# Kernel tuning notes

Hardware: AMD Instinct MI355X
Metric: run time of the kernel (lower is better)

Reference implementation:

```python
import jax, jax.numpy as jnp
import numpy as np

D_MODEL = 256
SEQ_L = 4096
BATCH = 8
H = 3 * D_MODEL   # inner width after 3-branch concat
N_STATE = 32      # complex conjugate pairs -> d_state=64 real
KSIZES = (3, 7, 15)
DILATIONS = (1, 2, 4)


def setup_inputs() -> dict:
    k = jax.random.split(jax.random.key(0), 16)
    d = D_MODEL
    def w(ki, shape, scale):
        return jax.random.normal(ki, shape, jnp.float32) * scale
    inp = {"x": jax.random.normal(k[0], (BATCH, SEQ_L, d), jnp.float32)}
    for i, ksz in enumerate(KSIZES):
        inp[f"conv_w{i}"] = w(k[1 + i], (d, d, ksz), (d * ksz) ** -0.5)
        inp[f"conv_b{i}"] = jnp.zeros((d,), jnp.float32)
    inp["gate_w"] = w(k[4], (H, d), d ** -0.5)
    inp["gate_b"] = jnp.zeros((H,), jnp.float32)
    inp["res_w"] = w(k[5], (H, d), d ** -0.5)
    inp["res_b"] = jnp.zeros((H,), jnp.float32)
    # S4D (diagonal SSM) parameters, d_state=64 -> 32 complex pairs
    inp["log_dt"] = jax.random.uniform(k[6], (H,), jnp.float32, np.log(0.001), np.log(0.1))
    inp["A_re"] = -0.5 * jnp.ones((H, N_STATE), jnp.float32)
    inp["A_im"] = jnp.broadcast_to(np.pi * jnp.arange(N_STATE, dtype=jnp.float32), (H, N_STATE)).copy()
    inp["C_re"] = w(k[7], (H, N_STATE), 0.2)
    inp["C_im"] = w(k[8], (H, N_STATE), 0.2)
    inp["Dskip"] = jax.random.normal(k[9], (H,), jnp.float32)
    inp["ln_gamma"] = jnp.ones((H,), jnp.float32)
    inp["ln_beta"] = jnp.zeros((H,), jnp.float32)
    return inp


def _dil_conv(u, w, b, dil):
    # u: [B, C, L], w: [O, I, K], torch 'same' padding (odd kernels)
    y = jax.lax.conv_general_dilated(
        u, w, window_strides=(1,), padding="SAME", rhs_dilation=(dil,),
        dimension_numbers=("NCH", "OIH", "NCH"))
    return y + b[None, :, None]


def _s4d_apply(u, log_dt, A_re, A_im, C_re, C_im, Dskip):
    # u: [B, H, L]; diagonal SSM long convolution via FFT (ZOH discretization)
    L = u.shape[-1]
    dt = jnp.exp(log_dt)                          # [H]
    A = A_re + 1j * A_im                          # [H, N]
    C = C_re + 1j * C_im                          # [H, N]
    dtA = dt[:, None] * A                         # [H, N]
    C_disc = C * (jnp.exp(dtA) - 1.0) / A         # ZOH input matrix folded into C
    t = jnp.arange(L, dtype=jnp.float32)
    vand = jnp.exp(dtA[:, :, None] * t)           # [H, N, L] Vandermonde
    kern = 2.0 * jnp.real(jnp.einsum("hn,hnl->hl", C_disc, vand))  # [H, L]
    n_fft = 2 * L
    kf = jnp.fft.rfft(kern, n_fft)                # [H, n_fft/2+1]
    uf = jnp.fft.rfft(u, n_fft)                   # [B, H, n_fft/2+1]
    y = jnp.fft.irfft(uf * kf[None], n_fft)[..., :L]
    return y + Dskip[None, :, None] * u


def reference(x, conv_w0, conv_b0, conv_w1, conv_b1, conv_w2, conv_b2,
              gate_w, gate_b, res_w, res_b,
              log_dt, A_re, A_im, C_re, C_im, Dskip, ln_gamma, ln_beta):
    u = jnp.transpose(x, (0, 2, 1))               # [B, d, L]
    convs = [
        _dil_conv(u, conv_w0, conv_b0, DILATIONS[0]),
        _dil_conv(u, conv_w1, conv_b1, DILATIONS[1]),
        _dil_conv(u, conv_w2, conv_b2, DILATIONS[2]),
    ]
    combined = jnp.concatenate(convs, axis=1)     # [B, 3d, L]
    gate = jax.nn.sigmoid(jnp.einsum("bdl,od->bol", u, gate_w) + gate_b[None, :, None])
    gated = combined * gate
    s4_out = _s4d_apply(gated, log_dt, A_re, A_im, C_re, C_im, Dskip)
    resid = jnp.einsum("bdl,od->bol", u, res_w) + res_b[None, :, None]
    out = jnp.transpose(s4_out + resid, (0, 2, 1))  # [B, L, 3d]
    mu = jnp.mean(out, axis=-1, keepdims=True)
    var = jnp.mean((out - mu) ** 2, axis=-1, keepdims=True)
    return (out - mu) * jax.lax.rsqrt(var + 1e-5) * ln_gamma + ln_beta
```

## Files before the change

kernel.cpp:

```cpp
#include <hip/hip_runtime.h>
#include <cstdint>
#include <cstddef>


#define B_ 8
#define L_ 4096
#define D_ 256
#define H_ 768
#define NST 32
#define LC 128
#define NC 32

typedef _Float16 f16;
typedef _Float16 f16x8 __attribute__((ext_vector_type(8)));
typedef _Float16 f16x4 __attribute__((ext_vector_type(4)));
typedef _Float16 f16x2 __attribute__((ext_vector_type(2)));
typedef float f32x4 __attribute__((ext_vector_type(4)));

__device__ __forceinline__ f32x4 mfma16(f16x8 a, f16x8 b, f32x4 c) {
  return __builtin_amdgcn_mfma_f32_16x16x32_f16(a, b, c, 0, 0, 0);
}

#define GLDS16(g, l)                                                              \
  __builtin_amdgcn_global_load_lds((const __attribute__((address_space(1))) void*)(g), \
                                   (__attribute__((address_space(3))) void*)(l), 16, 0, 0)

__global__ __launch_bounds__(256) void prep_all(
    const float* __restrict__ x, const float* __restrict__ gate_w,
    const float* __restrict__ res_w,
    const float* __restrict__ w0, const float* __restrict__ w1, const float* __restrict__ w2,
    f16* __restrict__ xh, f16* __restrict__ Ag, float* __restrict__ zbuf,
    f16* __restrict__ A) {
  __shared__ float ws_t[3840];
  int bid = blockIdx.x, tid = threadIdx.x;
  if (bid < 8192) {
    int i = (bid * 256 + tid) * 4;
    float4 v = *(const float4*)(x + i);
    f16x4 h; h[0]=(f16)v.x; h[1]=(f16)v.y; h[2]=(f16)v.z; h[3]=(f16)v.w;
    *(f16x4*)(xh + i) = h;
  } else if (bid < 8384) {
    int i = ((bid - 8192) * 256 + tid) * 4;
    float4 v = *(const float4*)(gate_w + i);
    f16x4 h; h[0]=(f16)v.x; h[1]=(f16)v.y; h[2]=(f16)v.z; h[3]=(f16)v.w;
    *(f16x4*)(Ag + i) = h;
  } else if (bid < 8576) {
    int i = ((bid - 8384) * 256 + tid) * 4;
    float4 v = *(const float4*)(res_w + i);
    f16* d = Ag + 768 * 256;
    f16x4 h; h[0]=(f16)v.x; h[1]=(f16)v.y; h[2]=(f16)v.z; h[3]=(f16)v.w;
    *(f16x4*)(d + i) = h;
  } else if (bid == 8576) {
    zbuf[tid] = 0.f;
  } else {
    int b2 = bid - 8577;
    int ci = b2 >> 8, o = b2 & 255;
    const float* w; int K, base;
    if (ci == 0)      { w = w0; K = 3;  base = 0; }
    else if (ci == 1) { w = w1; K = 7;  base = 256 * 768; }
    else              { w = w2; K = 15; base = 256 * 768 + 256 * 1792; }
    const float* wbase = w + (size_t)o * 256 * K;
    int n = 256 * K;
    for (int i = tid; i < n; i += 256) ws_t[i] = wbase[i];
    __syncthreads();
    f16* Ab = A + base + (size_t)o * 256 * K;
    for (int t = 0; t < K; ++t)
      Ab[t * 256 + tid] = (f16)ws_t[tid * K + t];
  }
}

__global__ __launch_bounds__(256) void s4_all(const float* __restrict__ log_dt,
                                              const float* __restrict__ A_re,
                                              const float* __restrict__ A_im,
                                              const float* __restrict__ C_re,
                                              const float* __restrict__ C_im,
                                              f16* __restrict__ A1, f16* __restrict__ A2,
                                              float* __restrict__ WLc,
                                              float* __restrict__ kT) {
  int bid = blockIdx.x, tid = threadIdx.x;
  if (bid < 96) {
    int idx = bid * 256 + tid;
    int h = idx >> 5, n = idx & 31;
    float dt = expf(log_dt[h]);
    float Ar = A_re[idx], Ai = A_im[idx];
    float ar = dt * Ar, ai = dt * Ai;
    float e = expf(ar), sn, cs; sincosf(ai, &sn, &cs);
    float wr = e * cs, wi = e * sn;
    float den = Ar * Ar + Ai * Ai;
    float Er = wr - 1.f, Ei = wi;
    float Cr = C_re[idx], Ci = C_im[idx];
    float nr = Cr * Er - Ci * Ei, ni = Cr * Ei + Ci * Er;
    float Cdr = (nr * Ar + ni * Ai) / den;
    float Cdi = (ni * Ar - nr * Ai) / den;
    f16* A1r = A1 + ((size_t)h * 64 + 2 * n) * LC;
    f16* A1i = A1 + ((size_t)h * 64 + 2 * n + 1) * LC;
    float pr = 1.f, pi = 0.f;
    for (int j = 0; j < LC; ++j) {
      A1r[LC - 1 - j] = (f16)pr; A1i[LC - 1 - j] = (f16)pi;
      float t0 = pr * wr - pi * wi; pi = pr * wi + pi * wr; pr = t0;
    }
    WLc[idx * 2] = pr; WLc[idx * 2 + 1] = pi;
    float qr = wr, qi = wi;
    for (int t = 0; t < LC; ++t) {
      A2[((size_t)h * LC + t) * 64 + 2 * n]     = (f16)(2.f * (Cdr * qr - Cdi * qi));
      A2[((size_t)h * LC + t) * 64 + 2 * n + 1] = (f16)(-2.f * (Cdr * qi + Cdi * qr));
      float t0 = qr * wr - qi * wi; qi = qr * wi + qi * wr; qr = t0;
    }
  } else {
    int idx = (bid - 96) * 256 + tid;
    int h = idx >> 7, j = idx & 127;
    float dt = expf(log_dt[h]);
    float acc = 0.f;
    for (int n = 0; n < NST; ++n) {
      float Ar = A_re[h * 32 + n], Ai = A_im[h * 32 + n];
      float ar = dt * Ar, ai = dt * Ai;
      float e1 = expf(ar), s1, c1; sincosf(ai, &s1, &c1);
      float wr = e1 * c1, wi = e1 * s1;
      float den = Ar * Ar + Ai * Ai;
      float Er = wr - 1.f, Ei = wi;
      float Cr = C_re[h * 32 + n], Ci = C_im[h * 32 + n];
      float nr = Cr * Er - Ci * Ei, ni = Cr * Ei + Ci * Er;
      float Cdr = (nr * Ar + ni * Ai) / den, Cdi = (ni * Ar - nr * Ai) / den;
      float ej = expf(ar * (float)j), sj, cj; sincosf(ai * (float)j, &sj, &cj);
      acc += 2.f * (Cdr * (ej * cj) - Cdi * (ej * sj));
    }
    kT[idx] = acc;
  }
}

__global__ __launch_bounds__(256) void gemm_gr(
    const f16* __restrict__ xh, const f16* __restrict__ Agr,
    const float* __restrict__ gate_b, const float* __restrict__ res_b,
    f16* __restrict__ gts, f16* __restrict__ res) {
  __shared__ f16 As[128 * 64];
  __shared__ f16 Bs[128 * 64];
  const int mt = blockIdx.y, nt = blockIdx.x;
  const int b = nt >> 5, l0 = (nt & 31) * 128;
  const bool isg = mt < 6;
  const int hbase = (isg ? mt : mt - 6) * 128;
  const f16* Abase = Agr + (size_t)((isg ? 0 : 768) + hbase) * 256;
  const int tid = threadIdx.x;
  const int wid = tid >> 6, lane = tid & 63, l15 = lane & 15, quad = lane >> 4;
  const int wm = (wid & 1) * 64, wn = (wid >> 1) * 64;
  const int srow = (wid << 5) + (lane >> 3);
  const int sperm = ((lane & 7) ^ (lane >> 3)) << 3;
  char* AsL = (char*)As + (wid << 12);
  char* BsL = (char*)Bs + (wid << 12);
  const f16* xrow = xh + (((size_t)b * L_) << 8);

  f32x4 acc[4][4];
#pragma unroll
  for (int i = 0; i < 4; ++i)
#pragma unroll
    for (int j = 0; j < 4; ++j) acc[i][j] = (f32x4){0.f, 0.f, 0.f, 0.f};

  for (int kc = 0; kc < 4; ++kc) {
#pragma unroll
    for (int j = 0; j < 4; ++j) {
      int row = srow + j * 8;
      GLDS16(Abase + (size_t)row * 256 + kc * 64 + sperm, AsL + (j << 10));
      GLDS16(xrow + ((size_t)(l0 + row) << 8) + kc * 64 + sperm, BsL + (j << 10));
    }
    __syncthreads();
#pragma unroll
    for (int k2 = 0; k2 < 2; ++k2) {
      f16x8 af[4], bf[4];
#pragma unroll
      for (int mi = 0; mi < 4; ++mi) {
        int r = wm + mi * 16 + l15;
        af[mi] = *(const f16x8*)(&As[r * 64 + (((k2 * 4 + quad) ^ (r & 7)) << 3)]);
      }
#pragma unroll
      for (int ni = 0; ni < 4; ++ni) {
        int r = wn + ni * 16 + l15;
        bf[ni] = *(const f16x8*)(&Bs[r * 64 + (((k2 * 4 + quad) ^ (r & 7)) << 3)]);
      }
#pragma unroll
      for (int mi = 0; mi < 4; ++mi)
#pragma unroll
        for (int ni = 0; ni < 4; ++ni) acc[mi][ni] = mfma16(af[mi], bf[ni], acc[mi][ni]);
    }
    __syncthreads();
  }

  if (isg) {
#pragma unroll
    for (int mi = 0; mi < 4; ++mi)
#pragma unroll
      for (int ni = 0; ni < 4; ++ni) {
        int hg = hbase + wm + mi * 16 + quad * 4;
        int lg = l0 + wn + ni * 16 + l15;
#pragma unroll
        for (int r = 0; r < 4; ++r) {
          float val = acc[mi][ni][r] + gate_b[hg + r];
          gts[((size_t)(b * H_ + hg + r)) * L_ + lg] = (f16)(1.f / (1.f + expf(-val)));
        }
      }
  } else {
#pragma unroll
    for (int mi = 0; mi < 4; ++mi)
#pragma unroll
      for (int ni = 0; ni < 4; ++ni) {
        int hg = hbase + wm + mi * 16 + quad * 4;
        int lg = l0 + wn + ni * 16 + l15;
#pragma unroll
        for (int r = 0; r < 4; ++r)
          res[((size_t)(b * H_ + hg + r)) * L_ + lg] = (f16)(acc[mi][ni][r] + res_b[hg + r]);
      }
  }
}

__global__ __launch_bounds__(512, 2) void gemm_conv8(
    const f16* __restrict__ xh, const f16* __restrict__ Aconv,
    const float* __restrict__ cb0, const float* __restrict__ cb1, const float* __restrict__ cb2,
    const f16* __restrict__ gts, const f16* __restrict__ zbuf,
    f16* __restrict__ v) {
  __shared__ f16 lds[69632];
  f16* Bs = lds + 49152;

  const int nt = blockIdx.x;
  const int b = nt >> 4, l0 = (nt & 15) * 256;
  const int ci = 2 - blockIdx.y;
  const int tid = threadIdx.x;
  const int wid = tid >> 6, lane = tid & 63, l15 = lane & 15, quad = lane >> 4;
  const int wr = wid >> 1, wc = wid & 1;
  const int rq = tid >> 3;
  const int cswz = ((tid & 7) ^ ((tid >> 3) & 7)) << 3;
  const f16* xrow = xh + (((size_t)b * L_) << 8);

  const f16* Acb; int Krow, taps, dil;
  if (ci == 0)      { Acb = Aconv;                          Krow = 768;  taps = 3;  dil = 1; }
  else if (ci == 1) { Acb = Aconv + 256 * 768;              Krow = 1792; taps = 7;  dil = 2; }
  else              { Acb = Aconv + 256 * 768 + 256 * 1792; Krow = 3840; taps = 15; dil = 4; }
  const int half = (taps - 1) / 2;
  const int shift0 = 32 - half * dil;

  f32x4 acc[4][8];
#pragma unroll
  for (int i = 0; i < 4; ++i)
#pragma unroll
    for (int j = 0; j < 8; ++j) acc[i][j] = (f32x4){0.f, 0.f, 0.f, 0.f};
  f16x8 af[4][2], bfA[2][2], bfB[2][2];

  auto stageB = [&](int jc) {
#pragma unroll
    for (int q = 0; q < 5; ++q) {
      int r = q * 64 + rq;
      int gl = l0 - 32 + r;
      const f16* src = (gl < 0 || gl >= L_) ? (zbuf + cswz)
                       : xrow + ((size_t)gl << 8) + jc * 64 + cswz;
      GLDS16(src, Bs + q * 4096 + wid * 512);
    }
  };
  auto stageA4 = [&](int t2, int jc2, f16* buf) {
#pragma unroll
    for (int q = 0; q < 4; ++q) {
      const f16* src = Acb + (size_t)(q * 64 + rq) * Krow + t2 * 256 + jc2 * 64 + cswz;
      GLDS16(src, buf + q * 4096 + wid * 512);
    }
  };
  auto readAF = [&](const f16* Ab) {
#pragma unroll
    for (int mi = 0; mi < 4; ++mi) {
      int r = wr * 64 + mi * 16 + l15;
#pragma unroll
      for (int k2 = 0; k2 < 2; ++k2)
        af[mi][k2] = *(const f16x8*)(Ab + r * 64 + (((k2 * 4 + quad) ^ (r & 7)) << 3));
    }
  };
  auto readBF = [&](int q, int shift, f16x8 (&bf)[2][2]) {
#pragma unroll
    for (int ni = 0; ni < 2; ++ni) {
      int r = shift + wc * 128 + q * 32 + ni * 16 + l15;
#pragma unroll
      for (int k2 = 0; k2 < 2; ++k2)
        bf[ni][k2] = *(const f16x8*)(Bs + r * 64 + (((k2 * 4 + quad) ^ (r & 7)) << 3));
    }
  };
  auto qMM = [&](int q, f16x8 (&bf)[2][2]) {
#pragma unroll
    for (int k2 = 0; k2 < 2; ++k2)
#pragma unroll
      for (int mi = 0; mi < 4; ++mi)
#pragma unroll
        for (int ni = 0; ni < 2; ++ni)
          acc[mi][q * 2 + ni] = mfma16(af[mi][k2], bf[ni][k2], acc[mi][q * 2 + ni]);
  };

  stageB(0);
  stageA4(0, 0, lds);
  stageA4(1, 0, lds + 16384);
  asm volatile("s_waitcnt vmcnt(0)" ::: "memory");
  __builtin_amdgcn_s_barrier();
  readBF(0, shift0, bfA);

  int ca = 0;
#pragma unroll 1
  for (int jc = 0; jc < 4; ++jc) {
#pragma unroll 1
    for (int t = 0; t < taps; ++t) {
      const int shift = shift0 + t * dil;
      f16* Acur = lds + ca * 16384;
      int pa = ca + 2; if (pa >= 3) pa -= 3;
      f16* Apre = lds + pa * 16384;
      int t2 = t + 2, jc2 = jc;
      if (t2 >= taps) { t2 -= taps; ++jc2; }
      const bool pf = (jc2 < 4);

      if (pf) stageA4(t2, jc2, Apre);
      readAF(Acur);
      readBF(1, shift, bfB);
      qMM(0, bfA);
      readBF(2, shift, bfA);
      qMM(1, bfB);
      readBF(3, shift, bfB);
      qMM(2, bfA);
      qMM(3, bfB);

      if (t < taps - 1) {
        readBF(0, shift + dil, bfA);
        if (pf) asm volatile("s_waitcnt vmcnt(4)" ::: "memory");
        else    asm volatile("s_waitcnt vmcnt(0)" ::: "memory");
        __builtin_amdgcn_s_barrier();
      } else if (jc < 3) {
        __builtin_amdgcn_s_barrier();
        stageB(jc + 1);
        asm volatile("s_waitcnt vmcnt(0)" ::: "memory");
        __builtin_amdgcn_s_barrier();
        readBF(0, shift0, bfA);
      }
      ca = (ca == 2) ? 0 : ca + 1;
    }
  }

  const float* cbias = (ci == 0) ? cb0 : (ci == 1 ? cb1 : cb2);
#pragma unroll
  for (int mi = 0; mi < 4; ++mi)
#pragma unroll
    for (int q = 0; q < 4; ++q)
#pragma unroll
      for (int ni = 0; ni < 2; ++ni) {
        int mg = wr * 64 + mi * 16 + quad * 4;
        int lg = l0 + wc * 128 + q * 32 + ni * 16 + l15;
        f32x4 a4 = acc[mi][q * 2 + ni];
#pragma unroll
        for (int r = 0; r < 4; ++r) {
          size_t a = ((size_t)(b * H_ + ci * 256 + mg + r)) * L_ + lg;
          float val = (a4[r] + cbias[mg + r]) * (float)gts[a];
          v[a] = (f16)val;
        }
      }
}

__global__ __launch_bounds__(256) void s1_states(const f16* __restrict__ v,
                                                 const f16* __restrict__ A1,
                                                 const float* __restrict__ WLc,
                                                 f16* __restrict__ Xin) {
  __shared__ f16 A1s[64 * 136];
  __shared__ f16 Vs[128 * 136];
  const int h = blockIdx.y, cb = blockIdx.x;
  const int tid = threadIdx.x;
  {
    int row = tid >> 2, q = tid & 3;
    const f16x8* src = (const f16x8*)(A1 + ((size_t)h * 64 + row) * 128 + q * 32);
    f16x8* dst = (f16x8*)(&A1s[row * 136 + q * 32]);
    dst[0] = src[0]; dst[1] = src[1]; dst[2] = src[2]; dst[3] = src[3];
  }
  {
    int col = tid >> 1, half = tid & 1;
    int cg = cb * 128 + col, b = cg >> 5, c = cg & 31;
    const f16x8* src = (const f16x8*)(v + ((size_t)(b * H_ + h)) * L_ + c * 128 + half * 64);
    f16x8* dst = (f16x8*)(&Vs[col * 136 + half * 64]);
    dst[0] = src[0]; dst[1] = src[1]; dst[2] = src[2]; dst[3] = src[3];
    dst[4] = src[4]; dst[5] = src[5]; dst[6] = src[6]; dst[7] = src[7];
  }
  __syncthreads();
  const int wid = tid >> 6, lane = tid & 63, l15 = lane & 15, quad = lane >> 4;
  const int n0 = wid * 32;
  f32x4 acc[4][2];
#pragma unroll
  for (int i = 0; i < 4; ++i) { acc[i][0] = (f32x4){0,0,0,0}; acc[i][1] = (f32x4){0,0,0,0}; }
#pragma unroll
  for (int bk = 0; bk < 4; ++bk) {
    f16x8 af[4], bf[2];
#pragma unroll
    for (int mi = 0; mi < 4; ++mi)
      af[mi] = *(const f16x8*)(&A1s[(mi * 16 + l15) * 136 + bk * 32 + quad * 8]);
#pragma unroll
    for (int ni = 0; ni < 2; ++ni)
      bf[ni] = *(const f16x8*)(&Vs[(n0 + ni * 16 + l15) * 136 + bk * 32 + quad * 8]);
#pragma unroll
    for (int mi = 0; mi < 4; ++mi)
#pragma unroll
      for (int ni = 0; ni < 2; ++ni) acc[mi][ni] = mfma16(af[mi], bf[ni], acc[mi][ni]);
  }
  __syncthreads();
  float* Xls = (float*)Vs;
#pragma unroll
  for (int mi = 0; mi < 4; ++mi)
#pragma unroll
    for (int ni = 0; ni < 2; ++ni) {
      int col = n0 + ni * 16 + l15;
      *(f32x4*)(&Xls[col * 68 + mi * 16 + quad * 4]) = acc[mi][ni];
    }
  __syncthreads();
  if (tid < 128) {
    int b4 = tid >> 5, n = tid & 31;
    int b = cb * 4 + b4;
    float Wr = WLc[(h * NST + n) * 2], Wi = WLc[(h * NST + n) * 2 + 1];
    float xr = 0.f, xi = 0.f;
    f16* xout = Xin + (((size_t)(b * H_ + h)) * NC) * 64 + 2 * n;
    for (int c = 0; c < NC; ++c) {
      float er = Xls[(b4 * 32 + c) * 68 + 2 * n];
      float ei = Xls[(b4 * 32 + c) * 68 + 2 * n + 1];
      f16x2 o; o[0] = (f16)xr; o[1] = (f16)xi;
      *(f16x2*)(xout + (size_t)c * 64) = o;
      float t = Wr * xr - Wi * xi + er;
      xi = Wr * xi + Wi * xr + ei; xr = t;
    }
  }
}

__global__ __launch_bounds__(256) void s3_output(const f16* __restrict__ v,
                                                 const f16* __restrict__ A2g,
                                                 const f16* __restrict__ res,
                                                 const float* __restrict__ kT,
                                                 const f16* __restrict__ Xin,
                                                 const float* __restrict__ Dskip,
                                                 f16* __restrict__ y4) {
  __shared__ f16 Ts[128 * 136];
  __shared__ f16 Vs[64 * 136];
  __shared__ float kTs[128];
  f16* A2s = Ts;
  f16* Xs = Ts + 128 * 72;
  const int h = blockIdx.y, cb = blockIdx.x;
  const int tid = threadIdx.x;
  if (tid < 128) kTs[tid] = kT[h * 128 + tid];
  {
    int col = tid >> 2, q = tid & 3;
    int cg = cb * 64 + col, b = cg >> 5, c = cg & 31;
    const f16x8* src = (const f16x8*)(v + ((size_t)(b * H_ + h)) * L_ + c * 128 + q * 32);
    f16x8* dst = (f16x8*)(&Vs[col * 136 + q * 32]);
    dst[0] = src[0]; dst[1] = src[1]; dst[2] = src[2]; dst[3] = src[3];
  }
  __syncthreads();
  {
    int tau = tid >> 1, h64 = (tid & 1) * 64;
#pragma unroll
    for (int jv = 0; jv < 8; ++jv) {
      int s0 = h64 + jv * 8;
      f16x8 w;
#pragma unroll
      for (int e = 0; e < 8; ++e) {
        int s = s0 + e;
        w[e] = (f16)((s <= tau) ? kTs[tau - s] : 0.f);
      }
      *(f16x8*)(&Ts[tau * 136 + s0]) = w;
    }
  }
  __syncthreads();
  const int wid = tid >> 6, lane = tid & 63, l15 = lane & 15, quad = lane >> 4;
  const int wm = (wid & 1) * 64, wn = (wid >> 1) * 32;
  f32x4 acc[4][2];
#pragma unroll
  for (int i = 0; i < 4; ++i) { acc[i][0] = (f32x4){0,0,0,0}; acc[i][1] = (f32x4){0,0,0,0}; }
#pragma unroll
  for (int bk = 0; bk < 4; ++bk) {
    f16x8 af[4], bf[2];
#pragma unroll
    for (int mi = 0; mi < 4; ++mi)
      af[mi] = *(const f16x8*)(&Ts[(wm + mi * 16 + l15) * 136 + bk * 32 + quad * 8]);
#pragma unroll
    for (int ni = 0; ni < 2; ++ni)
      bf[ni] = *(const f16x8*)(&Vs[(wn + ni * 16 + l15) * 136 + bk * 32 + quad * 8]);
#pragma unroll
    for (int mi = 0; mi < 4; ++mi)
#pragma unroll
      for (int ni = 0; ni < 2; ++ni) acc[mi][ni] = mfma16(af[mi], bf[ni], acc[mi][ni]);
  }
  __syncthreads();
  {
    int row = tid >> 1, half = tid & 1;
    const f16x8* src = (const f16x8*)(A2g + ((size_t)h * 128 + row) * 64 + half * 32);
    f16x8* dst = (f16x8*)(&A2s[row * 72 + half * 32]);
    dst[0] = src[0]; dst[1] = src[1]; dst[2] = src[2]; dst[3] = src[3];
  }
  {
    int col = tid >> 2, part = tid & 3;
    int cg = cb * 64 + col, b = cg >> 5, c = cg & 31;
    const f16x8* src = (const f16x8*)(Xin + (((size_t)(b * H_ + h)) * NC + c) * 64 + part * 16);
    f16x8* dst = (f16x8*)(&Xs[col * 72 + part * 16]);
    dst[0] = src[0]; dst[1] = src[1];
  }
  __syncthreads();
#pragma unroll
  for (int bk = 0; bk < 2; ++bk) {
    f16x8 af[4], bf[2];
#pragma unroll
    for (int mi = 0; mi < 4; ++mi)
      af[mi] = *(const f16x8*)(&A2s[(wm + mi * 16 + l15) * 72 + bk * 32 + quad * 8]);
#pragma unroll
    for (int ni = 0; ni < 2; ++ni)
      bf[ni] = *(const f16x8*)(&Xs[(wn + ni * 16 + l15) * 72 + bk * 32 + quad * 8]);
#pragma unroll
    for (int mi = 0; mi < 4; ++mi)
#pragma unroll
      for (int ni = 0; ni < 2; ++ni) acc[mi][ni] = mfma16(af[mi], bf[ni], acc[mi][ni]);
  }
  float Dh = Dskip[h];
#pragma unroll
  for (int mi = 0; mi < 4; ++mi)
#pragma unroll
    for (int ni = 0; ni < 2; ++ni) {
      int col = wn + ni * 16 + l15;
      int cg = cb * 64 + col, b = cg >> 5, c = cg & 31;
      int tau0 = wm + mi * 16 + quad * 4;
      size_t lbase = ((size_t)(b * H_ + h)) * L_ + c * 128 + tau0;
      const f16* rp = res + lbase;
      f16x4 o;
#pragma unroll
      for (int r = 0; r < 4; ++r)
        o[r] = (f16)(acc[mi][ni][r] + Dh * (float)Vs[col * 136 + tau0 + r] + (float)rp[r]);
      *(f16x4*)(y4 + lbase) = o;
    }
}

__global__ __launch_bounds__(256) void layernorm_t(const f16* __restrict__ y4,
                                                   const float* __restrict__ gamma,
                                                   const float* __restrict__ beta,
                                                   float* __restrict__ out) {
  __shared__ f16 Ys[768 * 66];
  __shared__ float psum[256], psq[256], mu[64], rs[64];
  const int b = blockIdx.y, l0 = blockIdx.x * 64;
  const int tid = threadIdx.x;
  {
    int r8 = tid >> 3, c = tid & 7;
    for (int it = 0; it < 24; ++it) {
      int hh = it * 32 + r8;
      f16x8 x = *(const f16x8*)(y4 + ((size_t)(b * H_ + hh)) * L_ + l0 + c * 8);
      *(f16x8*)(&Ys[hh * 66 + c * 8]) = x;
    }
  }
  __syncthreads();
  {
    int l = tid & 63, hg = tid >> 6;
    float s = 0.f, s2 = 0.f;
    for (int k = 0; k < 192; ++k) {
      float val = (float)Ys[(hg * 192 + k) * 66 + l];
      s += val; s2 += val * val;
    }
    psum[hg * 64 + l] = s; psq[hg * 64 + l] = s2;
  }
  __syncthreads();
  if (tid < 64) {
    float S = 0.f, S2 = 0.f;
    for (int g = 0; g < 4; ++g) { S += psum[g * 64 + tid]; S2 += psq[g * 64 + tid]; }
    float m = S / 768.f;
    float var = S2 / 768.f - m * m;
    mu[tid] = m; rs[tid] = rsqrtf(var + 1e-5f);
  }
  __syncthreads();
  float g0 = gamma[tid], g1 = gamma[256 + tid], g2 = gamma[512 + tid];
  float be0 = beta[tid], be1 = beta[256 + tid], be2 = beta[512 + tid];
  for (int lv = 0; lv < 8; ++lv) {
    f16x8 y0 = *(const f16x8*)(&Ys[(size_t)tid * 66 + lv * 8]);
    f16x8 y1 = *(const f16x8*)(&Ys[(size_t)(256 + tid) * 66 + lv * 8]);
    f16x8 y2 = *(const f16x8*)(&Ys[(size_t)(512 + tid) * 66 + lv * 8]);
#pragma unroll
    for (int e = 0; e < 8; ++e) {
      int ll = lv * 8 + e;
      float m = mu[ll], r = rs[ll];
      size_t ob = ((size_t)b * L_ + l0 + ll) * H_;
      out[ob + tid]       = ((float)y0[e] - m) * r * g0 + be0;
      out[ob + 256 + tid] = ((float)y1[e] - m) * r * g1 + be1;
      out[ob + 512 + tid] = ((float)y2[e] - m) * r * g2 + be2;
    }
  }
}

extern "C" void kernel_launch(void* const* d_in, const int* in_sizes, int n_in,
                              void* d_out, int out_size, void* d_ws, size_t ws_size,
                              hipStream_t stream) {
  const float* x      = (const float*)d_in[0];
  const float* cw0    = (const float*)d_in[1];
  const float* cb0    = (const float*)d_in[2];
  const float* cw1    = (const float*)d_in[3];
  const float* cb1    = (const float*)d_in[4];
  const float* cw2    = (const float*)d_in[5];
  const float* cb2    = (const float*)d_in[6];
  const float* gate_w = (const float*)d_in[7];
  const float* gate_b = (const float*)d_in[8];
  const float* res_w  = (const float*)d_in[9];
  const float* res_b  = (const float*)d_in[10];
  const float* log_dt = (const float*)d_in[11];
  const float* A_re   = (const float*)d_in[12];
  const float* A_im   = (const float*)d_in[13];
  const float* C_re   = (const float*)d_in[14];
  const float* C_im   = (const float*)d_in[15];
  const float* Dskip  = (const float*)d_in[16];
  const float* ln_g   = (const float*)d_in[17];
  const float* ln_b   = (const float*)d_in[18];
  float* out = (float*)d_out;

  char* ws = (char*)d_ws;
  f16*   xh   = (f16*)(ws + 0);
  f16*   Ac   = (f16*)(ws + 16777216);
  f16*   Ag   = (f16*)(ws + 20054016);
  f16*   zbuf = (f16*)(ws + 20840448);
  f16*   vb   = (f16*)(ws + 20841472);
  f16*   resb = (f16*)(ws + 71173120);
  f16*   gts  = (f16*)(ws + 121504768);
  f16*   A1   = (f16*)(ws + 171836416);
  f16*   A2   = (f16*)(ws + 184419328);
  float* kT   = (float*)(ws + 197002240);
  float* WLc  = (float*)(ws + 197395456);
  f16*   Xin  = (f16*)(ws + 197592064);
  f16*   y4   = (f16*)(ws + 222757888);

  prep_all<<<9345, 256, 0, stream>>>(x, gate_w, res_w, cw0, cw1, cw2,
                                     xh, Ag, (float*)zbuf, Ac);
  s4_all<<<480, 256, 0, stream>>>(log_dt, A_re, A_im, C_re, C_im, A1, A2, WLc, kT);

  gemm_gr<<<dim3(256, 12), 256, 0, stream>>>(xh, Ag, gate_b, res_b, gts, resb);
  gemm_conv8<<<dim3(128, 3), 512, 0, stream>>>(xh, Ac, cb0, cb1, cb2, gts, zbuf, vb);

  s1_states<<<dim3(2, 768), 256, 0, stream>>>(vb, A1, WLc, Xin);
  s3_output<<<dim3(4, 768), 256, 0, stream>>>(vb, A2, resb, kT, Xin, Dskip, y4);

  layernorm_t<<<dim3(64, 8), 256, 0, stream>>>(y4, ln_g, ln_b, out);
}
```

Before: 445.5 us.

## Fuse gate GEMM and sigmoid into conv GEMM kernel, drop gate buffer

Moves the gate projection GEMM out of gemm_gr and into the conv kernel. Each conv block first computes the gate tile for its own channels and positions, applies the sigmoid and keeps the result in registers as f16, then runs the conv taps and multiplies by the gate in its epilogue. This removes a write and a read of the B*H*L f16 gate tensor in global memory and halves the gemm_gr grid. The cost is extra registers per thread for the held gate values and a gate pre-pass with full barriers before the conv pipeline starts, which could hurt occupancy under launch_bounds(512,2).

```diff
diff --git a/kernel.cpp b/kernel.cpp
--- a/kernel.cpp
+++ b/kernel.cpp
@@ -129,15 +129,13 @@
 
 __global__ __launch_bounds__(256) void gemm_gr(
     const f16* __restrict__ xh, const f16* __restrict__ Agr,
-    const float* __restrict__ gate_b, const float* __restrict__ res_b,
-    f16* __restrict__ gts, f16* __restrict__ res) {
+    const float* __restrict__ res_b, f16* __restrict__ res) {
   __shared__ f16 As[128 * 64];
   __shared__ f16 Bs[128 * 64];
   const int mt = blockIdx.y, nt = blockIdx.x;
   const int b = nt >> 5, l0 = (nt & 31) * 128;
-  const bool isg = mt < 6;
-  const int hbase = (isg ? mt : mt - 6) * 128;
-  const f16* Abase = Agr + (size_t)((isg ? 0 : 768) + hbase) * 256;
+  const int hbase = mt * 128;
+  const f16* Abase = Agr + (size_t)(768 + hbase) * 256;
   const int tid = threadIdx.x;
   const int wid = tid >> 6, lane = tid & 63, l15 = lane & 15, quad = lane >> 4;
   const int wm = (wid & 1) * 64, wn = (wid >> 1) * 64;
@@ -182,37 +180,23 @@
     __syncthreads();
   }
 
-  if (isg) {
-#pragma unroll
-    for (int mi = 0; mi < 4; ++mi)
-#pragma unroll
-      for (int ni = 0; ni < 4; ++ni) {
-        int hg = hbase + wm + mi * 16 + quad * 4;
-        int lg = l0 + wn + ni * 16 + l15;
-#pragma unroll
-        for (int r = 0; r < 4; ++r) {
-          float val = acc[mi][ni][r] + gate_b[hg + r];
-          gts[((size_t)(b * H_ + hg + r)) * L_ + lg] = (f16)(1.f / (1.f + expf(-val)));
-        }
-      }
-  } else {
-#pragma unroll
-    for (int mi = 0; mi < 4; ++mi)
-#pragma unroll
-      for (int ni = 0; ni < 4; ++ni) {
-        int hg = hbase + wm + mi * 16 + quad * 4;
-        int lg = l0 + wn + ni * 16 + l15;
-#pragma unroll
-        for (int r = 0; r < 4; ++r)
-          res[((size_t)(b * H_ + hg + r)) * L_ + lg] = (f16)(acc[mi][ni][r] + res_b[hg + r]);
-      }
-  }
-}
-
-__global__ __launch_bounds__(512, 2) void gemm_conv8(
+#pragma unroll
+  for (int mi = 0; mi < 4; ++mi)
+#pragma unroll
+    for (int ni = 0; ni < 4; ++ni) {
+      int hg = hbase + wm + mi * 16 + quad * 4;
+      int lg = l0 + wn + ni * 16 + l15;
+#pragma unroll
+      for (int r = 0; r < 4; ++r)
+        res[((size_t)(b * H_ + hg + r)) * L_ + lg] = (f16)(acc[mi][ni][r] + res_b[hg + r]);
+    }
+}
+
+__global__ __launch_bounds__(512, 2) void gemm_convg(
     const f16* __restrict__ xh, const f16* __restrict__ Aconv,
+    const f16* __restrict__ Agate,
     const float* __restrict__ cb0, const float* __restrict__ cb1, const float* __restrict__ cb2,
-    const f16* __restrict__ gts, const f16* __restrict__ zbuf,
+    const float* __restrict__ gate_b, const f16* __restrict__ zbuf,
     f16* __restrict__ v) {
   __shared__ f16 lds[69632];
   f16* Bs = lds + 49152;
@@ -258,6 +242,13 @@
       GLDS16(src, buf + q * 4096 + wid * 512);
     }
   };
+  auto stageAg = [&](int jc2, f16* buf) {
+#pragma unroll
+    for (int q = 0; q < 4; ++q) {
+      const f16* src = Agate + (size_t)(ci * 256 + q * 64 + rq) * 256 + jc2 * 64 + cswz;
+      GLDS16(src, buf + q * 4096 + wid * 512);
+    }
+  };
   auto readAF = [&](const f16* Ab) {
 #pragma unroll
     for (int mi = 0; mi < 4; ++mi) {
@@ -286,7 +277,35 @@
           acc[mi][q * 2 + ni] = mfma16(af[mi][k2], bf[ni][k2], acc[mi][q * 2 + ni]);
   };
 
-  stageB(0);
+#pragma unroll 1
+  for (int u = 0; u < 4; ++u) {
+    int jcs = (u + 1) & 3;
+    stageB(jcs);
+    stageAg(jcs, lds);
+    asm volatile("s_waitcnt vmcnt(0)" ::: "memory");
+    __builtin_amdgcn_s_barrier();
+    readAF(lds);
+    readBF(0, 32, bfA); qMM(0, bfA);
+    readBF(1, 32, bfB); qMM(1, bfB);
+    readBF(2, 32, bfA); qMM(2, bfA);
+    readBF(3, 32, bfB); qMM(3, bfB);
+    __builtin_amdgcn_s_barrier();
+  }
+  f16x4 g4[4][8];
+#pragma unroll
+  for (int mi = 0; mi < 4; ++mi)
+#pragma unroll
+    for (int j = 0; j < 8; ++j) {
+      int mg = wr * 64 + mi * 16 + quad * 4;
+      f32x4 a4 = acc[mi][j];
+#pragma unroll
+      for (int r = 0; r < 4; ++r) {
+        float gv = a4[r] + gate_b[ci * 256 + mg + r];
+        g4[mi][j][r] = (f16)(1.f / (1.f + expf(-gv)));
+      }
+      acc[mi][j] = (f32x4){0.f, 0.f, 0.f, 0.f};
+    }
+
   stageA4(0, 0, lds);
   stageA4(1, 0, lds + 16384);
   asm volatile("s_waitcnt vmcnt(0)" ::: "memory");
@@ -345,7 +364,7 @@
 #pragma unroll
         for (int r = 0; r < 4; ++r) {
           size_t a = ((size_t)(b * H_ + ci * 256 + mg + r)) * L_ + lg;
-          float val = (a4[r] + cbias[mg + r]) * (float)gts[a];
+          float val = (a4[r] + cbias[mg + r]) * (float)g4[mi][q * 2 + ni][r];
           v[a] = (f16)val;
         }
       }
@@ -608,7 +627,6 @@
   f16*   zbuf = (f16*)(ws + 20840448);
   f16*   vb   = (f16*)(ws + 20841472);
   f16*   resb = (f16*)(ws + 71173120);
-  f16*   gts  = (f16*)(ws + 121504768);
   f16*   A1   = (f16*)(ws + 171836416);
   f16*   A2   = (f16*)(ws + 184419328);
   float* kT   = (float*)(ws + 197002240);
@@ -620,8 +638,9 @@
                                      xh, Ag, (float*)zbuf, Ac);
   s4_all<<<480, 256, 0, stream>>>(log_dt, A_re, A_im, C_re, C_im, A1, A2, WLc, kT);
 
-  gemm_gr<<<dim3(256, 12), 256, 0, stream>>>(xh, Ag, gate_b, res_b, gts, resb);
-  gemm_conv8<<<dim3(128, 3), 512, 0, stream>>>(xh, Ac, cb0, cb1, cb2, gts, zbuf, vb);
+  gemm_gr<<<dim3(256, 6), 256, 0, stream>>>(xh, Ag, res_b, resb);
+  gemm_convg<<<dim3(128, 3), 512, 0, stream>>>(xh, Ac, Ag, cb0, cb1, cb2,
+                                               gate_b, zbuf, vb);
 
   s1_states<<<dim3(2, 768), 256, 0, stream>>>(vb, A1, WLc, Xin);
   s3_output<<<dim3(4, 768), 256, 0, stream>>>(vb, A2, resb, kT, Xin, Dskip, y4);
```

Measured after the change: 466.5 us. +4.7%, slower.
